# Kernel tuning notes

Hardware: AMD Instinct MI355X
Metric: run time of the kernel (lower is better)

The kernel has to match this reference:

```python
import jax, jax.numpy as jnp
import numpy as np
import math

IN_SIZE = 512
OUT_SIZE = 512
N_HEADS = 8
D_K = OUT_SIZE // N_HEADS  # 64
N_NTYPES = 4
N_ETYPES = 8
MAX_LEN = 240
E = 150000


def _sinusoid_table():
    # RelTemporalEncoding fixed (non-trainable) embedding table [MAX_LEN, IN_SIZE]
    position = np.arange(0.0, MAX_LEN, dtype=np.float64)[:, None]
    div_term = np.exp(np.arange(0, IN_SIZE, 2, dtype=np.float64) * -(math.log(10000.0) / IN_SIZE))
    emb = np.zeros((MAX_LEN, IN_SIZE), dtype=np.float64)
    emb[:, 0::2] = np.sin(position * div_term) / IN_SIZE ** 0.5
    emb[:, 1::2] = np.cos(position * div_term) / IN_SIZE ** 0.5
    return jnp.asarray(emb, dtype=jnp.float32)


def typed_linear(x, types, W, b=None):
    """x: [E, ..., in], types: int[E], W: [T, out, in], b: [T, out] or None.
    Small fixed loop over T types with masked accumulation (avoids gathering a
    huge [E, out, in] weight tensor)."""
    out = jnp.zeros(x.shape[:-1] + (W.shape[1],), x.dtype)
    t_exp = types.reshape((-1,) + (1,) * (x.ndim - 1))
    for t in range(W.shape[0]):
        y = jnp.einsum('...i,oi->...o', x, W[t])
        if b is not None:
            y = y + b[t]
        out = out + jnp.where(t_exp == t, y, jnp.zeros((), x.dtype))
    return out


def setup_inputs() -> dict:
    key = jax.random.key(0)
    ks = jax.random.split(key, 12)
    xavier = lambda k, shape, fan_in, fan_out: jax.random.uniform(
        k, shape, jnp.float32, -1.0, 1.0) * math.sqrt(6.0 / (fan_in + fan_out))
    inp = {
        'h_s': jax.random.normal(ks[0], (E, IN_SIZE), jnp.float32),
        'Q_t': jax.random.normal(ks[1], (E, N_HEADS, D_K), jnp.float32),
        'etype': jax.random.randint(ks[2], (E,), 0, N_ETYPES),
        'tau_s': jax.random.randint(ks[3], (E,), 0, N_NTYPES),
        'dt': jax.random.randint(ks[4], (E,), 0, MAX_LEN),
        # RelTemporalEncoding params
        'emb': _sinusoid_table(),  # fixed, non-trainable
        'lin_W': xavier(ks[5], (IN_SIZE, IN_SIZE), IN_SIZE, IN_SIZE),
        'lin_b': jnp.zeros((IN_SIZE,), jnp.float32),
        # TypedLinear params (xavier_uniform like the torch code)
        'K_W': xavier(ks[6], (N_NTYPES, OUT_SIZE, IN_SIZE), IN_SIZE, OUT_SIZE),
        'K_b': jnp.zeros((N_NTYPES, OUT_SIZE), jnp.float32),
        'V_W': xavier(ks[7], (N_NTYPES, OUT_SIZE, IN_SIZE), IN_SIZE, OUT_SIZE),
        'V_b': jnp.zeros((N_NTYPES, OUT_SIZE), jnp.float32),
        'Watt_W': xavier(ks[8], (N_ETYPES, D_K, D_K), D_K, D_K),
        'Wmsg_W': xavier(ks[9], (N_ETYPES, D_K, D_K), D_K, D_K),
        'mu': jnp.ones((N_ETYPES, N_HEADS), jnp.float32),
    }
    return inp


def reference(h_s, Q_t, etype, tau_s, dt, emb, lin_W, lin_b,
              K_W, K_b, V_W, V_b, Watt_W, Wmsg_W, mu):
    n_edges = h_s.shape[0]
    # RelTemporalEncoding: x + Linear(emb[t])
    h_hat = h_s + emb[dt] @ lin_W.T + lin_b  # [E, in]
    # Typed K/V projections by source node type
    K_s = typed_linear(h_hat, tau_s, K_W, K_b).reshape(n_edges, N_HEADS, D_K)
    V_s = typed_linear(h_hat, tau_s, V_W, V_b).reshape(n_edges, N_HEADS, D_K)
    # Typed per-edge-type transforms
    M = typed_linear(V_s, etype, Wmsg_W)          # [E, H, d_k]
    att_head_k = typed_linear(K_s, etype, Watt_W)  # [E, H, d_k]
    att_head = (Q_t * att_head_k).sum(-1)          # [E, H]
    att_head = att_head * mu[etype] / D_K ** 0.5
    return att_head, M
```

## Files before the change

kernel.cpp:

```cpp
#include <hip/hip_runtime.h>
#include <hip/hip_bf16.h>
#include <stdint.h>

#define E_N 150000
#define IN 512
#define MAXLEN 240

#define PPERM 154112
#define NTILE2 1204
#define GRID_GEMM (NTILE2 * 8)

typedef __attribute__((ext_vector_type(8))) short short8;
typedef __attribute__((ext_vector_type(4))) float f32x4;

#define OFF_RB   0UL
#define OFF_W2   245760UL
#define OFF_B2   33800192UL
#define OFF_RW   33931264UL
#define OFF_CNT  65388544UL
#define OFF_PERM 65389056UL

static __device__ __forceinline__ short f2bf(float f) {
  union { float f; uint32_t u; } v; v.f = f;
  uint32_t u = v.u;
  uint32_t r = (u + 0x7fffu + ((u >> 16) & 1u)) >> 16;
  return (short)r;
}

static __device__ __forceinline__ uint32_t pk2(float a, float b) {
  union { __hip_bfloat162 h; uint32_t u; } v;
  v.h = __float22bfloat162_rn(make_float2(a, b));
  return v.u;
}

__global__ __launch_bounds__(256) void k_rte(const float* __restrict__ emb,
    const float* __restrict__ linW, const float* __restrict__ linB,
    short* __restrict__ Rbf) {
  __shared__ float x[IN];
  int p = blockIdx.x;
  for (int i = threadIdx.x; i < IN; i += 256) x[i] = emb[p * IN + i];
  __syncthreads();
  for (int o = threadIdx.x; o < IN; o += 256) {
    const float* w = linW + (long)o * IN;
    float s = 0.f;
#pragma unroll 4
    for (int k = 0; k < IN; k += 4) {
      float4 wv = *(const float4*)(w + k);
      s += wv.x * x[k] + wv.y * x[k + 1] + wv.z * x[k + 2] + wv.w * x[k + 3];
    }
    Rbf[p * IN + o] = f2bf(s + linB[o]);
  }
}

__global__ __launch_bounds__(256) void k_wpair(
    const float* __restrict__ WattW, const float* __restrict__ WmsgW,
    const float* __restrict__ KW, const float* __restrict__ VW,
    const float* __restrict__ Kb, const float* __restrict__ Vb,
    short* __restrict__ W2, float* __restrict__ B2) {
  __shared__ float Tl[64][65];
  int blk = blockIdx.x;
  int p = blk >> 4, s = blk & 15;
  int t = p >> 3, g = p & 7;
  bool kside = s < 8;
  int h = kside ? s : s - 8;
  const float* T = (kside ? WattW : WmsgW) + (size_t)g * 4096;
  const float* S = (kside ? KW : VW) + ((size_t)t * 512 + h * 64) * 512;
  const float* bsrc = (kside ? Kb : Vb) + t * 512 + h * 64;
  int tid = threadIdx.x;
  for (int i = tid; i < 4096; i += 256) Tl[i >> 6][i & 63] = T[i];
  __syncthreads();
  int op = tid & 63, iq = tid >> 6;
  size_t obase = ((size_t)p * 1024 + (kside ? 0 : 512) + h * 64 + op) * 512;
  for (int i8 = 0; i8 < 16; i8++) {
    int i0 = iq * 128 + i8 * 8;
    float a0 = 0, a1 = 0, a2 = 0, a3 = 0, a4 = 0, a5 = 0, a6 = 0, a7 = 0;
    const float* sp0 = S + i0;
#pragma unroll 8
    for (int j = 0; j < 64; j++) {
      float tv = Tl[op][j];
      const float* sp = sp0 + j * 512;
      float4 s0 = *(const float4*)sp;
      float4 s1 = *(const float4*)(sp + 4);
      a0 += tv * s0.x; a1 += tv * s0.y; a2 += tv * s0.z; a3 += tv * s0.w;
      a4 += tv * s1.x; a5 += tv * s1.y; a6 += tv * s1.z; a7 += tv * s1.w;
    }
    short8 o8;
    o8[0] = f2bf(a0); o8[1] = f2bf(a1); o8[2] = f2bf(a2); o8[3] = f2bf(a3);
    o8[4] = f2bf(a4); o8[5] = f2bf(a5); o8[6] = f2bf(a6); o8[7] = f2bf(a7);
    *(short8*)(W2 + obase + i0) = o8;
  }
  if (tid < 64) {
    float b = 0;
#pragma unroll 8
    for (int j = 0; j < 64; j++) b += Tl[tid][j] * bsrc[j];
    B2[p * 1024 + (kside ? 0 : 512) + h * 64 + tid] = b;
  }
}

__global__ __launch_bounds__(256, 4) void k_rw2(
    const short* __restrict__ Rbf, const short* __restrict__ W2,
    const float* __restrict__ B2, float* __restrict__ RW) {
  __shared__ short sA[4096];
  __shared__ short sB[4096];
  int tid = threadIdx.x;
  int bid = blockIdx.x;
  int p = bid >> 4, rt = (bid >> 3) & 1, ctile = bid & 7;
  int n0 = ctile * 128;
  int r0 = rt * 128;

  int lane = tid & 63, w = tid >> 6, wm = w >> 1, wn = w & 1;

  int rS = w * 32 + (lane >> 2);
  int cS = lane & 3;
  int ch0 = (cS - (rS >> 1)) & 3;
  int ch1 = (cS - ((rS + 16) >> 1)) & 3;
  const char* rbb = (const char*)Rbf;
  const char* srcA0 = rbb + (size_t)(r0 + rS) * 1024 + ch0 * 16;
  const char* srcA1 = rbb + (size_t)(r0 + rS + 16) * 1024 + ch1 * 16;
  const char* wcb = (const char*)(W2 + ((size_t)p * 1024 + n0) * 512);
  const char* srcB0 = wcb + (size_t)rS * 1024 + ch0 * 16;
  const char* srcB1 = wcb + (size_t)(rS + 16) * 1024 + ch1 * 16;
  char* dA0 = (char*)sA + w * 2048;
  char* dA1 = (char*)sA + w * 2048 + 1024;
  char* dB0 = (char*)sB + w * 2048;
  char* dB1 = (char*)sB + w * 2048 + 1024;

  int aRow = wm * 64 + (lane & 15);
  int aOff = aRow * 64 + ((((lane >> 4) + (aRow >> 1)) & 3) << 4);
  int bRow = wn * 64 + (lane & 15);
  int bOff = bRow * 64 + ((((lane >> 4) + (bRow >> 1)) & 3) << 4);

  f32x4 acc[4][4] = {};
#pragma unroll
  for (int kk = 0; kk < 16; kk++) {
    __syncthreads();
    __builtin_amdgcn_global_load_lds((const uint32_t*)(srcA0 + kk * 64), (uint32_t*)dA0, 16, 0, 0);
    __builtin_amdgcn_global_load_lds((const uint32_t*)(srcA1 + kk * 64), (uint32_t*)dA1, 16, 0, 0);
    __builtin_amdgcn_global_load_lds((const uint32_t*)(srcB0 + kk * 64), (uint32_t*)dB0, 16, 0, 0);
    __builtin_amdgcn_global_load_lds((const uint32_t*)(srcB1 + kk * 64), (uint32_t*)dB1, 16, 0, 0);
    __syncthreads();
    short8 a[4], b[4];
#pragma unroll
    for (int mi = 0; mi < 4; mi++)
      a[mi] = *(const short8*)((const char*)sA + aOff + mi * 1024);
#pragma unroll
    for (int ni = 0; ni < 4; ni++)
      b[ni] = *(const short8*)((const char*)sB + bOff + ni * 1024);
#pragma unroll
    for (int mi = 0; mi < 4; mi++)
#pragma unroll
      for (int ni = 0; ni < 4; ni++)
        acc[mi][ni] = __builtin_amdgcn_mfma_f32_16x16x32_bf16(a[mi], b[ni], acc[mi][ni], 0, 0, 0);
  }

  int l15 = lane & 15;
  int rbase = (lane >> 4) * 4;
  float bias[4];
#pragma unroll
  for (int ni = 0; ni < 4; ni++)
    bias[ni] = B2[p * 1024 + n0 + wn * 64 + ni * 16 + l15];
#pragma unroll
  for (int mi = 0; mi < 4; mi++) {
#pragma unroll
    for (int r = 0; r < 4; r++) {
      int row = r0 + wm * 64 + mi * 16 + rbase + r;
      if (row >= MAXLEN) continue;
      float* dst = RW + ((size_t)p * 240 + row) * 1024 + n0 + wn * 64;
#pragma unroll
      for (int ni = 0; ni < 4; ni++)
        dst[ni * 16 + l15] = acc[mi][ni][r] + bias[ni];
    }
  }
}

__global__ __launch_bounds__(256) void k_hist(const int* __restrict__ tau,
    const int* __restrict__ et, int* __restrict__ cnt) {
  __shared__ int l[32];
  if (threadIdx.x < 32) l[threadIdx.x] = 0;
  __syncthreads();
  int e = blockIdx.x * 256 + threadIdx.x;
  if (e < E_N) atomicAdd(&l[tau[e] * 8 + et[e]], 1);
  __syncthreads();
  if (threadIdx.x < 32) atomicAdd(&cnt[threadIdx.x], l[threadIdx.x]);
}

__global__ void k_bases(int* c) {
  int b = 0;
  for (int p = 0; p < 32; p++) {
    c[32 + p] = b;
    b += ((c[p] + 127) >> 7) << 7;
    c[64 + p] = 0;
  }
}

__global__ __launch_bounds__(256) void k_scatter(const int* __restrict__ tau,
    const int* __restrict__ et, int* __restrict__ c, int* __restrict__ perm) {
  __shared__ int lc[32], lbase[32];
  if (threadIdx.x < 32) lc[threadIdx.x] = 0;
  __syncthreads();
  int e = blockIdx.x * 256 + threadIdx.x;
  bool v = e < E_N;
  int cls = 0, pos = 0;
  if (v) {
    cls = tau[e] * 8 + et[e];
    pos = atomicAdd(&lc[cls], 1);
  }
  __syncthreads();
  if (threadIdx.x < 32) {
    int n = lc[threadIdx.x];
    lbase[threadIdx.x] = (n > 0) ? atomicAdd(&c[64 + threadIdx.x], n) : 0;
  }
  __syncthreads();
  if (v) perm[c[32 + cls] + lbase[cls] + pos] = e;
}

__global__ __launch_bounds__(256, 4) void k_gemm(
    const float* __restrict__ hs, const int* __restrict__ dt,
    const int* __restrict__ tau, const int* __restrict__ et,
    const short* __restrict__ W2, const float* __restrict__ RW,
    const float* __restrict__ Qt, const float* __restrict__ mu,
    const int* __restrict__ perm,
    float* __restrict__ Mout, float* __restrict__ attOut) {
  __shared__ short sA[4096];
  __shared__ short sB[4096];
  __shared__ int eRow[128];
  __shared__ int dtRow[128];
  __shared__ int metaP;
  int tid = threadIdx.x;
  int l = (blockIdx.x & 7) * NTILE2 + (blockIdx.x >> 3);
  int ttile = l >> 3, ctile = l & 7;
  int m0 = ttile * 128;
  if (tid < 128) {
    int e = perm[m0 + tid];
    eRow[tid] = e;
    dtRow[tid] = (e >= 0) ? dt[e] : 0;
  }
  if (tid == 0) {
    int e0 = perm[m0];
    metaP = (e0 >= 0) ? (tau[e0] * 8 + et[e0]) : -1;
  }
  __syncthreads();
  int p = metaP;
  if (p < 0) return;
  int n0 = ctile * 128;

  int lane = tid & 63, w = tid >> 6, wm = w >> 1, wn = w & 1;

  int arow = tid >> 1;
  int ahalf = tid & 1;
  long aE = eRow[arow]; if (aE < 0) aE = 0;
  const float* asrc = hs + aE * 512 + ahalf * 16;
  int swzA = (arow >> 1) & 3;
  int c0 = ahalf * 2;
  char* wA0 = (char*)sA + arow * 64 + (((c0    ) + swzA) & 3) * 16;
  char* wA1 = (char*)sA + arow * 64 + (((c0 + 1) + swzA) & 3) * 16;

  int rS = w * 32 + (lane >> 2);
  int cS = lane & 3;
  int ch0 = (cS - (rS >> 1)) & 3;
  int ch1 = (cS - ((rS + 16) >> 1)) & 3;
  const char* wcb = (const char*)(W2 + ((size_t)p * 1024 + n0) * 512);
  const char* srcB0 = wcb + (size_t)rS * 1024 + ch0 * 16;
  const char* srcB1 = wcb + (size_t)(rS + 16) * 1024 + ch1 * 16;
  char* dB0 = (char*)sB + w * 2048;
  char* dB1 = (char*)sB + w * 2048 + 1024;

  int aRowF = wm * 64 + (lane & 15);
  int aOff = aRowF * 64 + ((((lane >> 4) + (aRowF >> 1)) & 3) << 4);
  int bRow = wn * 64 + (lane & 15);
  int bOff = bRow * 64 + ((((lane >> 4) + (bRow >> 1)) & 3) << 4);

  f32x4 acc[4][4] = {};
  float4 pf0 = *(const float4*)(asrc);
  float4 pf1 = *(const float4*)(asrc + 4);
  float4 pf2 = *(const float4*)(asrc + 8);
  float4 pf3 = *(const float4*)(asrc + 12);
#pragma unroll
  for (int kk = 0; kk < 16; kk++) {
    __syncthreads();
    union { short8 s; uint32_t u[4]; } w0, w1;
    w0.u[0] = pk2(pf0.x, pf0.y); w0.u[1] = pk2(pf0.z, pf0.w);
    w0.u[2] = pk2(pf1.x, pf1.y); w0.u[3] = pk2(pf1.z, pf1.w);
    w1.u[0] = pk2(pf2.x, pf2.y); w1.u[1] = pk2(pf2.z, pf2.w);
    w1.u[2] = pk2(pf3.x, pf3.y); w1.u[3] = pk2(pf3.z, pf3.w);
    *(short8*)wA0 = w0.s;
    *(short8*)wA1 = w1.s;
    __builtin_amdgcn_global_load_lds((const uint32_t*)(srcB0 + kk * 64), (uint32_t*)dB0, 16, 0, 0);
    __builtin_amdgcn_global_load_lds((const uint32_t*)(srcB1 + kk * 64), (uint32_t*)dB1, 16, 0, 0);
    if (kk < 15) {
      const float* np = asrc + (kk + 1) * 32;
      pf0 = *(const float4*)(np);
      pf1 = *(const float4*)(np + 4);
      pf2 = *(const float4*)(np + 8);
      pf3 = *(const float4*)(np + 12);
    }
    __syncthreads();
    short8 a[4], b[4];
#pragma unroll
    for (int mi = 0; mi < 4; mi++)
      a[mi] = *(const short8*)((const char*)sA + aOff + mi * 1024);
#pragma unroll
    for (int ni = 0; ni < 4; ni++)
      b[ni] = *(const short8*)((const char*)sB + bOff + ni * 1024);
#pragma unroll
    for (int mi = 0; mi < 4; mi++)
#pragma unroll
      for (int ni = 0; ni < 4; ni++)
        acc[mi][ni] = __builtin_amdgcn_mfma_f32_16x16x32_bf16(a[mi], b[ni], acc[mi][ni], 0, 0, 0);
  }

  int l15 = lane & 15;
  int rbase = (lane >> 4) * 4;
  if (ctile < 4) {
    int h = ctile * 2 + wn;
    float muv = mu[(p & 7) * 8 + h] * 0.125f;
#pragma unroll
    for (int mi = 0; mi < 4; mi++) {
#pragma unroll
      for (int r = 0; r < 4; r++) {
        int row = wm * 64 + mi * 16 + rbase + r;
        int e = eRow[row];
        if (e < 0) continue;
        const float* rw = RW + ((size_t)p * 240 + dtRow[row]) * 1024 + n0 + wn * 64;
        const float* qp = Qt + (size_t)e * 512 + h * 64;
        float s = 0.f;
#pragma unroll
        for (int ni = 0; ni < 4; ni++)
          s += qp[ni * 16 + l15] * (acc[mi][ni][r] + rw[ni * 16 + l15]);
        s += __shfl_xor(s, 1);
        s += __shfl_xor(s, 2);
        s += __shfl_xor(s, 4);
        s += __shfl_xor(s, 8);
        if (l15 == 0) attOut[(size_t)e * 8 + h] = s * muv;
      }
    }
  } else {
#pragma unroll
    for (int mi = 0; mi < 4; mi++) {
#pragma unroll
      for (int r = 0; r < 4; r++) {
        int row = wm * 64 + mi * 16 + rbase + r;
        int e = eRow[row];
        if (e < 0) continue;
        const float* rw = RW + ((size_t)p * 240 + dtRow[row]) * 1024 + n0 + wn * 64;
        float* md = Mout + (size_t)e * 512 + (n0 - 512) + wn * 64;
#pragma unroll
        for (int ni = 0; ni < 4; ni++)
          md[ni * 16 + l15] = acc[mi][ni][r] + rw[ni * 16 + l15];
      }
    }
  }
}

extern "C" void kernel_launch(void* const* d_in, const int* in_sizes, int n_in,
                              void* d_out, int out_size, void* d_ws, size_t ws_size,
                              hipStream_t stream) {
  const float* hs    = (const float*)d_in[0];
  const float* Qt    = (const float*)d_in[1];
  const int*   et    = (const int*)d_in[2];
  const int*   tau   = (const int*)d_in[3];
  const int*   dt    = (const int*)d_in[4];
  const float* emb   = (const float*)d_in[5];
  const float* linW  = (const float*)d_in[6];
  const float* linB  = (const float*)d_in[7];
  const float* KW    = (const float*)d_in[8];
  const float* Kb    = (const float*)d_in[9];
  const float* VW    = (const float*)d_in[10];
  const float* Vb    = (const float*)d_in[11];
  const float* WattW = (const float*)d_in[12];
  const float* WmsgW = (const float*)d_in[13];
  const float* mu    = (const float*)d_in[14];

  char* ws = (char*)d_ws;
  short* Rbf  = (short*)(ws + OFF_RB);
  short* W2   = (short*)(ws + OFF_W2);
  float* B2   = (float*)(ws + OFF_B2);
  float* RW   = (float*)(ws + OFF_RW);
  int*   cnt  = (int*)(ws + OFF_CNT);
  int*   perm = (int*)(ws + OFF_PERM);

  float* attOut = (float*)d_out;
  float* Mout   = (float*)d_out + (long)E_N * 8;

  hipMemsetAsync(cnt, 0, 128 * sizeof(int), stream);
  hipMemsetAsync(perm, 0xFF, PPERM * sizeof(int), stream);

  k_rte<<<240, 256, 0, stream>>>(emb, linW, linB, Rbf);
  k_wpair<<<512, 256, 0, stream>>>(WattW, WmsgW, KW, VW, Kb, Vb, W2, B2);
  k_hist<<<(E_N + 255) / 256, 256, 0, stream>>>(tau, et, cnt);
  k_bases<<<1, 1, 0, stream>>>(cnt);
  k_scatter<<<(E_N + 255) / 256, 256, 0, stream>>>(tau, et, cnt, perm);
  k_rw2<<<512, 256, 0, stream>>>(Rbf, W2, B2, RW);
  k_gemm<<<GRID_GEMM, 256, 0, stream>>>(hs, dt, tau, et, W2, RW, Qt, mu, perm, Mout, attOut);
}
```

Baseline: 717.5 us.

## Double-buffer LDS tiles in main GEMM and split weight-pair kernel across more blocks

The main GEMM kernel now keeps two LDS buffers for the A and B tiles. It stages the next k-slice (async global-to-LDS for B, convert-and-store for A) while running MFMAs on the current slice, which cuts the two barriers per iteration down to one. Occupancy is lowered from 4 to 3 blocks per SIMD target to allow for the doubled shared memory. Separately, the weight-pair precompute kernel is split four ways along the input dimension (2048 blocks instead of 512) to expose more parallelism, at the cost of each block reloading the 64x64 transform into LDS.

Result: faster. 696.4 us (-2.9%).

```diff
diff --git a/kernel.cpp b/kernel.cpp
--- a/kernel.cpp
+++ b/kernel.cpp
@@ -59,7 +59,7 @@
     short* __restrict__ W2, float* __restrict__ B2) {
   __shared__ float Tl[64][65];
   int blk = blockIdx.x;
-  int p = blk >> 4, s = blk & 15;
+  int p = blk >> 6, s = (blk >> 2) & 15, q = blk & 3;
   int t = p >> 3, g = p & 7;
   bool kside = s < 8;
   int h = kside ? s : s - 8;
@@ -71,7 +71,7 @@
   __syncthreads();
   int op = tid & 63, iq = tid >> 6;
   size_t obase = ((size_t)p * 1024 + (kside ? 0 : 512) + h * 64 + op) * 512;
-  for (int i8 = 0; i8 < 16; i8++) {
+  for (int i8 = q * 4; i8 < q * 4 + 4; i8++) {
     int i0 = iq * 128 + i8 * 8;
     float a0 = 0, a1 = 0, a2 = 0, a3 = 0, a4 = 0, a5 = 0, a6 = 0, a7 = 0;
     const float* sp0 = S + i0;
@@ -89,7 +89,7 @@
     o8[4] = f2bf(a4); o8[5] = f2bf(a5); o8[6] = f2bf(a6); o8[7] = f2bf(a7);
     *(short8*)(W2 + obase + i0) = o8;
   }
-  if (tid < 64) {
+  if (q == 0 && tid < 64) {
     float b = 0;
 #pragma unroll 8
     for (int j = 0; j < 64; j++) b += Tl[tid][j] * bsrc[j];
@@ -214,15 +214,15 @@
   if (v) perm[c[32 + cls] + lbase[cls] + pos] = e;
 }
 
-__global__ __launch_bounds__(256, 4) void k_gemm(
+__global__ __launch_bounds__(256, 3) void k_gemm(
     const float* __restrict__ hs, const int* __restrict__ dt,
     const int* __restrict__ tau, const int* __restrict__ et,
     const short* __restrict__ W2, const float* __restrict__ RW,
     const float* __restrict__ Qt, const float* __restrict__ mu,
     const int* __restrict__ perm,
     float* __restrict__ Mout, float* __restrict__ attOut) {
-  __shared__ short sA[4096];
-  __shared__ short sB[4096];
+  __shared__ short sA[2][4096];
+  __shared__ short sB[2][4096];
   __shared__ int eRow[128];
   __shared__ int dtRow[128];
   __shared__ int metaP;
@@ -252,8 +252,8 @@
   const float* asrc = hs + aE * 512 + ahalf * 16;
   int swzA = (arow >> 1) & 3;
   int c0 = ahalf * 2;
-  char* wA0 = (char*)sA + arow * 64 + (((c0    ) + swzA) & 3) * 16;
-  char* wA1 = (char*)sA + arow * 64 + (((c0 + 1) + swzA) & 3) * 16;
+  int aw0 = arow * 64 + (((c0    ) + swzA) & 3) * 16;
+  int aw1 = arow * 64 + (((c0 + 1) + swzA) & 3) * 16;
 
   int rS = w * 32 + (lane >> 2);
   int cS = lane & 3;
@@ -262,52 +262,61 @@
   const char* wcb = (const char*)(W2 + ((size_t)p * 1024 + n0) * 512);
   const char* srcB0 = wcb + (size_t)rS * 1024 + ch0 * 16;
   const char* srcB1 = wcb + (size_t)(rS + 16) * 1024 + ch1 * 16;
-  char* dB0 = (char*)sB + w * 2048;
-  char* dB1 = (char*)sB + w * 2048 + 1024;
 
   int aRowF = wm * 64 + (lane & 15);
   int aOff = aRowF * 64 + ((((lane >> 4) + (aRowF >> 1)) & 3) << 4);
   int bRow = wn * 64 + (lane & 15);
   int bOff = bRow * 64 + ((((lane >> 4) + (bRow >> 1)) & 3) << 4);
 
+  float4 pf0, pf1, pf2, pf3;
+#define LOADPF(k) { const float* np = asrc + (k) * 32; \
+    pf0 = *(const float4*)(np); pf1 = *(const float4*)(np + 4); \
+    pf2 = *(const float4*)(np + 8); pf3 = *(const float4*)(np + 12); }
+#define CVTWRITE(buf) { union { short8 s; uint32_t u[4]; } w0_, w1_; \
+    w0_.u[0] = pk2(pf0.x, pf0.y); w0_.u[1] = pk2(pf0.z, pf0.w); \
+    w0_.u[2] = pk2(pf1.x, pf1.y); w0_.u[3] = pk2(pf1.z, pf1.w); \
+    w1_.u[0] = pk2(pf2.x, pf2.y); w1_.u[1] = pk2(pf2.z, pf2.w); \
+    w1_.u[2] = pk2(pf3.x, pf3.y); w1_.u[3] = pk2(pf3.z, pf3.w); \
+    *(short8*)((char*)sA[buf] + aw0) = w0_.s; \
+    *(short8*)((char*)sA[buf] + aw1) = w1_.s; }
+#define STAGEB(k, buf) { \
+    __builtin_amdgcn_global_load_lds((const uint32_t*)(srcB0 + (k) * 64), \
+        (uint32_t*)((char*)sB[buf] + w * 2048), 16, 0, 0); \
+    __builtin_amdgcn_global_load_lds((const uint32_t*)(srcB1 + (k) * 64), \
+        (uint32_t*)((char*)sB[buf] + w * 2048 + 1024), 16, 0, 0); }
+
   f32x4 acc[4][4] = {};
-  float4 pf0 = *(const float4*)(asrc);
-  float4 pf1 = *(const float4*)(asrc + 4);
-  float4 pf2 = *(const float4*)(asrc + 8);
-  float4 pf3 = *(const float4*)(asrc + 12);
+  LOADPF(0);
+  STAGEB(0, 0);
+  CVTWRITE(0);
+  LOADPF(1);
+  __syncthreads();
+
 #pragma unroll
   for (int kk = 0; kk < 16; kk++) {
-    __syncthreads();
-    union { short8 s; uint32_t u[4]; } w0, w1;
-    w0.u[0] = pk2(pf0.x, pf0.y); w0.u[1] = pk2(pf0.z, pf0.w);
-    w0.u[2] = pk2(pf1.x, pf1.y); w0.u[3] = pk2(pf1.z, pf1.w);
-    w1.u[0] = pk2(pf2.x, pf2.y); w1.u[1] = pk2(pf2.z, pf2.w);
-    w1.u[2] = pk2(pf3.x, pf3.y); w1.u[3] = pk2(pf3.z, pf3.w);
-    *(short8*)wA0 = w0.s;
-    *(short8*)wA1 = w1.s;
-    __builtin_amdgcn_global_load_lds((const uint32_t*)(srcB0 + kk * 64), (uint32_t*)dB0, 16, 0, 0);
-    __builtin_amdgcn_global_load_lds((const uint32_t*)(srcB1 + kk * 64), (uint32_t*)dB1, 16, 0, 0);
+    int cur = kk & 1, nxt = cur ^ 1;
     if (kk < 15) {
-      const float* np = asrc + (kk + 1) * 32;
-      pf0 = *(const float4*)(np);
-      pf1 = *(const float4*)(np + 4);
-      pf2 = *(const float4*)(np + 8);
-      pf3 = *(const float4*)(np + 12);
-    }
-    __syncthreads();
+      STAGEB(kk + 1, nxt);
+      CVTWRITE(nxt);
+      if (kk < 14) LOADPF(kk + 2);
+    }
     short8 a[4], b[4];
 #pragma unroll
     for (int mi = 0; mi < 4; mi++)
-      a[mi] = *(const short8*)((const char*)sA + aOff + mi * 1024);
+      a[mi] = *(const short8*)((const char*)sA[cur] + aOff + mi * 1024);
 #pragma unroll
     for (int ni = 0; ni < 4; ni++)
-      b[ni] = *(const short8*)((const char*)sB + bOff + ni * 1024);
+      b[ni] = *(const short8*)((const char*)sB[cur] + bOff + ni * 1024);
 #pragma unroll
     for (int mi = 0; mi < 4; mi++)
 #pragma unroll
       for (int ni = 0; ni < 4; ni++)
         acc[mi][ni] = __builtin_amdgcn_mfma_f32_16x16x32_bf16(a[mi], b[ni], acc[mi][ni], 0, 0, 0);
-  }
+    __syncthreads();
+  }
+#undef LOADPF
+#undef CVTWRITE
+#undef STAGEB
 
   int l15 = lane & 15;
   int rbase = (lane >> 4) * 4;
@@ -386,7 +395,7 @@
   hipMemsetAsync(perm, 0xFF, PPERM * sizeof(int), stream);
 
   k_rte<<<240, 256, 0, stream>>>(emb, linW, linB, Rbf);
-  k_wpair<<<512, 256, 0, stream>>>(WattW, WmsgW, KW, VW, Kb, Vb, W2, B2);
+  k_wpair<<<2048, 256, 0, stream>>>(WattW, WmsgW, KW, VW, Kb, Vb, W2, B2);
   k_hist<<<(E_N + 255) / 256, 256, 0, stream>>>(tau, et, cnt);
   k_bases<<<1, 1, 0, stream>>>(cnt);
   k_scatter<<<(E_N + 255) / 256, 256, 0, stream>>>(tau, et, cnt, perm);
```
